# Kernel tuning notes

Hardware: AMD Instinct MI355X
Metric: run time of the kernel (lower is better)

The kernel has to match this reference:

```python
import jax, jax.numpy as jnp
import numpy as np

N = 50000      # nodes
E = 600000     # edges
IN = 128       # in_channels
H = 128        # hidden_channels
CH = 32        # chunk_size
L = 3          # num_layers
G = 64         # num graphs in batch
EPS = 1e-5


def layer_norm(x, gamma, beta):
    mu = jnp.mean(x, axis=-1, keepdims=True)
    var = jnp.mean(jnp.square(x - mu), axis=-1, keepdims=True)
    return (x - mu) * jax.lax.rsqrt(var + EPS) * gamma + beta


def setup_inputs() -> dict:
    key = jax.random.key(0)
    ks = jax.random.split(key, 8)
    x = jax.random.normal(ks[0], (N, IN), dtype=jnp.float32)
    edge_index = jax.random.randint(ks[1], (2, E), 0, N, dtype=jnp.int64)
    batch = jnp.sort(jax.random.randint(ks[2], (N,), 0, G, dtype=jnp.int64))
    W_in = jax.random.normal(ks[3], (IN, H), dtype=jnp.float32) / np.sqrt(IN)
    b_in = jnp.zeros((H,), jnp.float32)
    ln_in_g = jnp.ones((H,), jnp.float32)
    ln_in_b = jnp.zeros((H,), jnp.float32)
    # shared (global_gating=True) tm_net: Linear(2H -> chunk_size)
    W_tm = jax.random.normal(ks[4], (2 * H, CH), dtype=jnp.float32) / np.sqrt(2 * H)
    b_tm = jnp.zeros((CH,), jnp.float32)
    tm_g = jnp.ones((L, H), jnp.float32)   # per-layer tm_norm gamma
    tm_b = jnp.zeros((L, H), jnp.float32)  # per-layer tm_norm beta
    return {"x": x, "edge_index": edge_index, "batch": batch,
            "W_in": W_in, "b_in": b_in, "ln_in_g": ln_in_g, "ln_in_b": ln_in_b,
            "W_tm": W_tm, "b_tm": b_tm, "tm_g": tm_g, "tm_b": tm_b}


def reference(x, edge_index, batch, W_in, b_in, ln_in_g, ln_in_b, W_tm, b_tm, tm_g, tm_b):
    # Input MLP (dropout is identity in eval)
    h = layer_norm(jax.nn.relu(x @ W_in + b_in), ln_in_g, ln_in_b)  # [N,H]

    src, dst = edge_index[0], edge_index[1]
    valid = (src != dst).astype(h.dtype)  # remove self loops
    r = H // CH
    # degree after remove_self_loops + add_self_loops (+1 for the self loop)
    deg = jax.ops.segment_sum(valid, dst, num_segments=N) + 1.0  # [N]

    tm = jnp.zeros((N, CH), h.dtype)  # last_tm_signal
    for j in range(L):
        # scatter-mean message passing with self loops
        msg = h[src] * valid[:, None]                        # [E,H]
        agg = jax.ops.segment_sum(msg, dst, num_segments=N)  # [N,H]
        m = (agg + h) / deg[:, None]
        # ordered gating: softmax -> cumsum -> diff-or with previous signal
        raw = jax.nn.softmax(jnp.concatenate([h, m], axis=1) @ W_tm + b_tm, axis=-1)
        raw = jnp.cumsum(raw, axis=-1)
        raw = tm + (1.0 - tm) * raw                          # [N,CH]
        sig = jnp.repeat(raw, r, axis=1)                     # [N,H]
        h = layer_norm(h * sig + m * (1.0 - sig), tm_g[j], tm_b[j])
        tm = raw

    # global mean pool over graphs
    counts = jax.ops.segment_sum(jnp.ones((N,), h.dtype), batch, num_segments=G)
    pooled = jax.ops.segment_sum(h, batch, num_segments=G) / jnp.maximum(counts, 1.0)[:, None]
    return pooled  # [G,H]
```

## Files before the change

kernel.cpp:

```cpp
#include <hip/hip_runtime.h>

#define NN 50000
#define NE 600000
#define HC 128
#define CHN 32
#define NG 64
#define LN_EPS 1e-5f

typedef unsigned short ushort_t;
typedef unsigned int uint_t;
typedef _Float16 half2_t __attribute__((ext_vector_type(2)));

__device__ __forceinline__ ushort_t f2h(float f) {
    _Float16 h = (_Float16)f;
    return __builtin_bit_cast(ushort_t, h);
}
__device__ __forceinline__ float h2f(ushort_t s) {
    _Float16 h = __builtin_bit_cast(_Float16, s);
    return (float)h;
}
__device__ __forceinline__ uint_t pkh(float e, float o) {
    return (uint_t)f2h(e) | ((uint_t)f2h(o) << 16);
}
__device__ __forceinline__ float dot2h(uint_t a, uint_t b, float c) {
#if __has_builtin(__builtin_amdgcn_fdot2)
    return __builtin_amdgcn_fdot2(__builtin_bit_cast(half2_t, a),
                                  __builtin_bit_cast(half2_t, b), c, false);
#else
    half2_t ha = __builtin_bit_cast(half2_t, a);
    half2_t hb = __builtin_bit_cast(half2_t, b);
    c = fmaf((float)ha.x, (float)hb.x, c);
    c = fmaf((float)ha.y, (float)hb.y, c);
    return c;
#endif
}


__global__ void __launch_bounds__(256) k_hist(const int* __restrict__ ei, int* __restrict__ cnt) {
    int e = blockIdx.x * 256 + threadIdx.x;
    if (e >= NE) return;
    int s = ei[e], d = ei[NE + e];
    if (s != d) atomicAdd(&cnt[d], 1);
}

#define SC_BLOCKS 49

__global__ void __launch_bounds__(256) k_scanA(const int* __restrict__ cnt, int* __restrict__ blocksum) {
    int b = blockIdx.x, t = threadIdx.x;
    int idx = b * 1024 + t * 4;
    int4 v = make_int4(0, 0, 0, 0);
    if (idx + 3 < NN) v = *(const int4*)&cnt[idx];
    else {
        if (idx + 0 < NN) v.x = cnt[idx + 0];
        if (idx + 1 < NN) v.y = cnt[idx + 1];
        if (idx + 2 < NN) v.z = cnt[idx + 2];
        if (idx + 3 < NN) v.w = cnt[idx + 3];
    }
    int s = v.x + v.y + v.z + v.w;
    for (int m = 1; m < 64; m <<= 1) s += __shfl_xor(s, m, 64);
    __shared__ int ws[4];
    if ((t & 63) == 0) ws[t >> 6] = s;
    __syncthreads();
    if (t == 0) blocksum[b] = ws[0] + ws[1] + ws[2] + ws[3];
}

__global__ void __launch_bounds__(64) k_scanB(const int* __restrict__ blocksum, int* __restrict__ blockoff) {
    int t = threadIdx.x;
    int v = (t < SC_BLOCKS) ? blocksum[t] : 0;
    int inc = v;
    for (int d = 1; d < 64; d <<= 1) { int u = __shfl_up(inc, d, 64); if (t >= d) inc += u; }
    if (t < SC_BLOCKS) blockoff[t + 1] = inc;
    if (t == 0) blockoff[0] = 0;
}

__global__ void __launch_bounds__(256) k_scanC(const int* __restrict__ cnt, const int* __restrict__ blockoff,
                                               int* __restrict__ row_ptr) {
    int b = blockIdx.x, t = threadIdx.x;
    int idx = b * 1024 + t * 4;
    int4 v = make_int4(0, 0, 0, 0);
    if (idx + 3 < NN) v = *(const int4*)&cnt[idx];
    else {
        if (idx + 0 < NN) v.x = cnt[idx + 0];
        if (idx + 1 < NN) v.y = cnt[idx + 1];
        if (idx + 2 < NN) v.z = cnt[idx + 2];
        if (idx + 3 < NN) v.w = cnt[idx + 3];
    }
    int s = v.x + v.y + v.z + v.w;
    int lane = t & 63, w = t >> 6;
    int inc = s;
    for (int d = 1; d < 64; d <<= 1) { int u = __shfl_up(inc, d, 64); if (lane >= d) inc += u; }
    __shared__ int wsum[4];
    if (lane == 63) wsum[w] = inc;
    __syncthreads();
    int off = blockoff[b];
    for (int i = 0; i < w; ++i) off += wsum[i];
    int excl = off + inc - s;
    if (idx + 0 < NN) row_ptr[idx + 0] = excl;
    if (idx + 1 < NN) row_ptr[idx + 1] = excl + v.x;
    if (idx + 2 < NN) row_ptr[idx + 2] = excl + v.x + v.y;
    if (idx + 3 < NN) row_ptr[idx + 3] = excl + v.x + v.y + v.z;
    if (b == 0 && t == 0) row_ptr[NN] = blockoff[SC_BLOCKS];
}

__global__ void __launch_bounds__(256) k_fill(const int* __restrict__ ei, const int* __restrict__ row_ptr,
                                              int* __restrict__ fill, int* __restrict__ col) {
    int e = blockIdx.x * 256 + threadIdx.x;
    if (e >= NE) return;
    int s = ei[e], d = ei[NE + e];
    if (s != d) {
        int pos = atomicAdd(&fill[d], 1);
        col[row_ptr[d] + pos] = s;
    }
}


__global__ void __launch_bounds__(256) k_prepW(const float* __restrict__ Wtm, uint_t* __restrict__ Wg) {
    int i = blockIdx.x * 256 + threadIdx.x;
    if (i >= (HC / 2) * 2 * CHN) return;
    int cp = i >> 5, kk = i & 31;
    Wg[i] = pkh(Wtm[(2 * cp) * CHN + kk], Wtm[(2 * cp + 1) * CHN + kk]);
}


#define MLP_NB 8
#define MLP_GROUPS (NN / MLP_NB)

__global__ void __launch_bounds__(256) k_mlp(const float* __restrict__ x, const float* __restrict__ W,
                                             const float* __restrict__ b, const float* __restrict__ g,
                                             const float* __restrict__ be, ushort_t* __restrict__ h2) {
    __shared__ float xs[4][MLP_NB][HC];
    int tid = threadIdx.x;
    int wave = tid >> 6, lane = tid & 63;
    float bx = b[2 * lane],  by = b[2 * lane + 1];
    float gx = g[2 * lane],  gy = g[2 * lane + 1];
    float bex = be[2 * lane], bey = be[2 * lane + 1];
    for (int grp = blockIdx.x * 4 + wave; grp < MLP_GROUPS; grp += gridDim.x * 4) {
        int base = grp * MLP_NB;
        #pragma unroll
        for (int nb = 0; nb < MLP_NB; ++nb) {
            float2 xv = *(const float2*)&x[(size_t)(base + nb) * HC + 2 * lane];
            *(float2*)&xs[wave][nb][2 * lane] = xv;
        }
        float ax[MLP_NB], ay[MLP_NB];
        #pragma unroll
        for (int nb = 0; nb < MLP_NB; ++nb) { ax[nb] = bx; ay[nb] = by; }
        for (int c = 0; c < HC; c += 4) {
            float2 wv0 = *(const float2*)&W[(c + 0) * HC + 2 * lane];
            float2 wv1 = *(const float2*)&W[(c + 1) * HC + 2 * lane];
            float2 wv2 = *(const float2*)&W[(c + 2) * HC + 2 * lane];
            float2 wv3 = *(const float2*)&W[(c + 3) * HC + 2 * lane];
            #pragma unroll
            for (int nb = 0; nb < MLP_NB; ++nb) {
                float4 xv = *(const float4*)&xs[wave][nb][c];
                ax[nb] = fmaf(xv.x, wv0.x, ax[nb]); ay[nb] = fmaf(xv.x, wv0.y, ay[nb]);
                ax[nb] = fmaf(xv.y, wv1.x, ax[nb]); ay[nb] = fmaf(xv.y, wv1.y, ay[nb]);
                ax[nb] = fmaf(xv.z, wv2.x, ax[nb]); ay[nb] = fmaf(xv.z, wv2.y, ay[nb]);
                ax[nb] = fmaf(xv.w, wv3.x, ax[nb]); ay[nb] = fmaf(xv.w, wv3.y, ay[nb]);
            }
        }
        #pragma unroll
        for (int nb = 0; nb < MLP_NB; ++nb) {
            float a0 = fmaxf(ax[nb], 0.f), a1 = fmaxf(ay[nb], 0.f);
            float sm = a0 + a1;
            for (int m = 1; m < 64; m <<= 1) sm += __shfl_xor(sm, m, 64);
            float mu = sm * (1.f / 128.f);
            float d0 = a0 - mu, d1 = a1 - mu;
            float vv = d0 * d0 + d1 * d1;
            for (int m = 1; m < 64; m <<= 1) vv += __shfl_xor(vv, m, 64);
            float inv = rsqrtf(vv * (1.f / 128.f) + LN_EPS);
            float ox = d0 * inv * gx + bex;
            float oy = d1 * inv * gy + bey;
            *(uint_t*)&h2[(size_t)(base + nb) * HC + 2 * lane] = pkh(ox, oy);
        }
    }
}


__global__ void __launch_bounds__(256) k_flayer(
        const ushort_t* __restrict__ h2in, ushort_t* __restrict__ h2out,
        const int* __restrict__ row_ptr, const int* __restrict__ col,
        const uint_t* __restrict__ Wg, const float* __restrict__ btm,
        const float* __restrict__ gall, const float* __restrict__ ball,
        float* __restrict__ tm, int layer) {
    __shared__ uint_t hm_pk[4][2][64];
    int tid = threadIdx.x;
    int wave = tid >> 6, lane = tid & 63;
    int k = lane & 31, half = lane >> 5;
    int node = blockIdx.x * 4 + wave;
    int r0 = row_ptr[node], r1 = row_ptr[node + 1];
    int deg = r1 - r0;
    float tmo = tm[(size_t)node * CHN + k];
    float bk  = btm[k];
    float gx  = gall[layer * HC + 2 * lane], gy  = gall[layer * HC + 2 * lane + 1];
    float bex = ball[layer * HC + 2 * lane], bey = ball[layer * HC + 2 * lane + 1];
    half2_t acc = (half2_t)(_Float16)0;
    for (int base = 0; base < deg; base += 64) {
        int nIdx = min(64, deg - base);
        int myc = (base + lane < deg) ? col[r0 + base + lane] : 0;
        int j = 0;
        for (; j + 4 <= nIdx; j += 4) {
            int s0 = __shfl(myc, j,     64);
            int s1 = __shfl(myc, j + 1, 64);
            int s2 = __shfl(myc, j + 2, 64);
            int s3 = __shfl(myc, j + 3, 64);
            uint_t v0 = *(const uint_t*)&h2in[(size_t)s0 * HC + 2 * lane];
            uint_t v1 = *(const uint_t*)&h2in[(size_t)s1 * HC + 2 * lane];
            uint_t v2 = *(const uint_t*)&h2in[(size_t)s2 * HC + 2 * lane];
            uint_t v3 = *(const uint_t*)&h2in[(size_t)s3 * HC + 2 * lane];
            acc += __builtin_bit_cast(half2_t, v0);
            acc += __builtin_bit_cast(half2_t, v1);
            acc += __builtin_bit_cast(half2_t, v2);
            acc += __builtin_bit_cast(half2_t, v3);
        }
        for (; j < nIdx; ++j) {
            int s = __shfl(myc, j, 64);
            uint_t v = *(const uint_t*)&h2in[(size_t)s * HC + 2 * lane];
            acc += __builtin_bit_cast(half2_t, v);
        }
    }
    float ax = (float)acc.x, ay = (float)acc.y;
    uint_t hvp = *(const uint_t*)&h2in[(size_t)node * HC + 2 * lane];
    float h0 = h2f((ushort_t)(hvp & 0xFFFFu)), h1 = h2f((ushort_t)(hvp >> 16));
    float invdeg = 1.f / (float)(deg + 1);
    float m0 = (ax + h0) * invdeg, m1 = (ay + h1) * invdeg;
    hm_pk[wave][0][lane] = hvp;
    hm_pk[wave][1][lane] = pkh(m0, m1);
    const uint_t* sp = &hm_pk[wave][half][0];
    const uint_t* wp = Wg + (size_t)(half * 64) * CHN + k;
    float z = 0.f;
    #pragma unroll
    for (int i = 0; i < 16; ++i) {
        uint4 s4 = *(const uint4*)&sp[4 * i];
        uint_t w0 = wp[(4 * i + 0) * CHN];
        uint_t w1 = wp[(4 * i + 1) * CHN];
        uint_t w2 = wp[(4 * i + 2) * CHN];
        uint_t w3 = wp[(4 * i + 3) * CHN];
        z = dot2h(s4.x, w0, z);
        z = dot2h(s4.y, w1, z);
        z = dot2h(s4.z, w2, z);
        z = dot2h(s4.w, w3, z);
    }
    z += __shfl_xor(z, 32, 64);
    z += bk;
    float mx = z;
    for (int m = 1; m < 32; m <<= 1) mx = fmaxf(mx, __shfl_xor(mx, m, 32));
    float e = __expf(z - mx);
    float se = e;
    for (int m = 1; m < 32; m <<= 1) se += __shfl_xor(se, m, 32);
    float p = e / se;
    float cum = p;
    for (int d = 1; d < 32; d <<= 1) {
        float t2 = __shfl_up(cum, d, 32);
        if (k >= d) cum += t2;
    }
    float raw = tmo + (1.f - tmo) * cum;
    if (half == 0) tm[(size_t)node * CHN + k] = raw;
    float sig = __shfl(raw, lane >> 1, 64);
    float v0 = h0 * sig + m0 * (1.f - sig);
    float v1 = h1 * sig + m1 * (1.f - sig);
    float sm = v0 + v1;
    for (int m = 1; m < 64; m <<= 1) sm += __shfl_xor(sm, m, 64);
    float mu = sm * (1.f / 128.f);
    float d0 = v0 - mu, d1 = v1 - mu;
    float vv = d0 * d0 + d1 * d1;
    for (int m = 1; m < 64; m <<= 1) vv += __shfl_xor(vv, m, 64);
    float inv = rsqrtf(vv * (1.f / 128.f) + LN_EPS);
    *(uint_t*)&h2out[(size_t)node * HC + 2 * lane] = pkh(d0 * inv * gx + bex,
                                                         d1 * inv * gy + bey);
}


__global__ void __launch_bounds__(1024) k_pool(const ushort_t* __restrict__ h2, const int* __restrict__ batch,
                                               float* __restrict__ out) {
    __shared__ float red[8][HC];
    int g = blockIdx.x;
    int tid = threadIdx.x;
    int c = tid & (HC - 1);
    int w = tid >> 7;
    int a = 0, bnd = NN;
    while (a < bnd) { int mid = (a + bnd) >> 1; if (batch[mid] < g) a = mid + 1; else bnd = mid; }
    int start = a;
    bnd = NN;
    while (a < bnd) { int mid = (a + bnd) >> 1; if (batch[mid] <= g) a = mid + 1; else bnd = mid; }
    int end = a;
    float acc = 0.f;
    for (int n = start + w; n < end; n += 8) acc += h2f(h2[(size_t)n * HC + c]);
    red[w][c] = acc;
    __syncthreads();
    if (w == 0) {
        float s = red[0][c] + red[1][c] + red[2][c] + red[3][c]
                + red[4][c] + red[5][c] + red[6][c] + red[7][c];
        int count = end - start;
        out[g * HC + c] = s / (float)max(count, 1);
    }
}


extern "C" void kernel_launch(void* const* d_in, const int* in_sizes, int n_in,
                              void* d_out, int out_size, void* d_ws, size_t ws_size,
                              hipStream_t stream) {
    const float* x     = (const float*)d_in[0];
    const int*   ei    = (const int*)d_in[1];
    const int*   batch = (const int*)d_in[2];
    const float* W_in  = (const float*)d_in[3];
    const float* b_in  = (const float*)d_in[4];
    const float* g_in  = (const float*)d_in[5];
    const float* be_in = (const float*)d_in[6];
    const float* W_tm  = (const float*)d_in[7];
    const float* b_tm  = (const float*)d_in[8];
    const float* tm_g  = (const float*)d_in[9];
    const float* tm_b  = (const float*)d_in[10];
    float* out = (float*)d_out;

    char* ws = (char*)d_ws;
    int*      cnt = (int*)(ws + 0);
    int*      fil = (int*)(ws + 200000);
    int*      rp  = (int*)(ws + 400000);
    int*      col = (int*)(ws + 600004);
    ushort_t* h2A = (ushort_t*)(ws + 3000064);
    ushort_t* h2B = (ushort_t*)(ws + 15800064);
    float*    tm  = (float*)(ws + 28600064);
    int*      bsum = (int*)(ws + 35000064);
    int*      boff = (int*)(ws + 35000320);
    uint_t*   Wg   = (uint_t*)(ws + 35000576);

    hipMemsetAsync(cnt, 0, 400000, stream);
    hipMemsetAsync(tm, 0, 6400000, stream);

    k_hist<<<(NE + 255) / 256, 256, 0, stream>>>(ei, cnt);
    k_scanA<<<SC_BLOCKS, 256, 0, stream>>>(cnt, bsum);
    k_scanB<<<1, 64, 0, stream>>>(bsum, boff);
    k_scanC<<<SC_BLOCKS, 256, 0, stream>>>(cnt, boff, rp);
    k_fill<<<(NE + 255) / 256, 256, 0, stream>>>(ei, rp, fil, col);
    k_prepW<<<16, 256, 0, stream>>>(W_tm, Wg);

    k_mlp<<<1563, 256, 0, stream>>>(x, W_in, b_in, g_in, be_in, h2A);

    k_flayer<<<NN / 4, 256, 0, stream>>>(h2A, h2B, rp, col, Wg, b_tm, tm_g, tm_b, tm, 0);
    k_flayer<<<NN / 4, 256, 0, stream>>>(h2B, h2A, rp, col, Wg, b_tm, tm_g, tm_b, tm, 1);
    k_flayer<<<NN / 4, 256, 0, stream>>>(h2A, h2B, rp, col, Wg, b_tm, tm_g, tm_b, tm, 2);

    k_pool<<<NG, 1024, 0, stream>>>(h2B, batch, out);
}
```

Baseline: 300.4 us.

## Split wave into two edge halves with 8-byte gathers, fp16 gating state, fused memsets

```diff
diff --git a/kernel.cpp b/kernel.cpp
--- a/kernel.cpp
+++ b/kernel.cpp
@@ -21,6 +21,9 @@
 }
 __device__ __forceinline__ uint_t pkh(float e, float o) {
     return (uint_t)f2h(e) | ((uint_t)f2h(o) << 16);
+}
+__device__ __forceinline__ half2_t bch(uint_t u) {
+    return __builtin_bit_cast(half2_t, u);
 }
 __device__ __forceinline__ float dot2h(uint_t a, uint_t b, float c) {
 #if __has_builtin(__builtin_amdgcn_fdot2)
@@ -114,11 +117,14 @@
 }
 
 
-__global__ void __launch_bounds__(256) k_prepW(const float* __restrict__ Wtm, uint_t* __restrict__ Wg) {
+__global__ void __launch_bounds__(256) k_prep(const float* __restrict__ Wtm, uint_t* __restrict__ Wg,
+                                              int* __restrict__ cnt) {
     int i = blockIdx.x * 256 + threadIdx.x;
-    if (i >= (HC / 2) * 2 * CHN) return;
-    int cp = i >> 5, kk = i & 31;
-    Wg[i] = pkh(Wtm[(2 * cp) * CHN + kk], Wtm[(2 * cp + 1) * CHN + kk]);
+    if (i < 32 * 128) {
+        int cp = i >> 5, kk = i & 31;
+        Wg[i] = pkh(Wtm[(2 * cp) * CHN + kk], Wtm[(2 * cp + 1) * CHN + kk]);
+    }
+    for (int z = i; z < 2 * NN; z += gridDim.x * 256) cnt[z] = 0;
 }
 
 
@@ -127,7 +133,10 @@
 
 __global__ void __launch_bounds__(256) k_mlp(const float* __restrict__ x, const float* __restrict__ W,
                                              const float* __restrict__ b, const float* __restrict__ g,
-                                             const float* __restrict__ be, ushort_t* __restrict__ h2) {
+                                             const float* __restrict__ be, ushort_t* __restrict__ h2,
+                                             ushort_t* __restrict__ tm) {
+    uint_t* tz = (uint_t*)tm;
+    for (int z = blockIdx.x * 256 + threadIdx.x; z < NN * CHN / 2; z += gridDim.x * 256) tz[z] = 0u;
     __shared__ float xs[4][MLP_NB][HC];
     int tid = threadIdx.x;
     int wave = tid >> 6, lane = tid & 63;
@@ -181,52 +190,67 @@
         const int* __restrict__ row_ptr, const int* __restrict__ col,
         const uint_t* __restrict__ Wg, const float* __restrict__ btm,
         const float* __restrict__ gall, const float* __restrict__ ball,
-        float* __restrict__ tm, int layer) {
+        ushort_t* __restrict__ tm, int layer) {
     __shared__ uint_t hm_pk[4][2][64];
     int tid = threadIdx.x;
     int wave = tid >> 6, lane = tid & 63;
-    int k = lane & 31, half = lane >> 5;
+    int l32 = lane & 31, half = lane >> 5;
     int node = blockIdx.x * 4 + wave;
     int r0 = row_ptr[node], r1 = row_ptr[node + 1];
     int deg = r1 - r0;
-    float tmo = tm[(size_t)node * CHN + k];
-    float bk  = btm[k];
-    float gx  = gall[layer * HC + 2 * lane], gy  = gall[layer * HC + 2 * lane + 1];
-    float bex = ball[layer * HC + 2 * lane], bey = ball[layer * HC + 2 * lane + 1];
-    half2_t acc = (half2_t)(_Float16)0;
+    float tmo = h2f(tm[(size_t)node * CHN + l32]);
+    float bk  = btm[l32];
+    float4 gv = *(const float4*)&gall[layer * HC + 4 * l32];
+    float4 bv = *(const float4*)&ball[layer * HC + 4 * l32];
+    half2_t acc0 = (half2_t)(_Float16)0, acc1 = (half2_t)(_Float16)0;
     for (int base = 0; base < deg; base += 64) {
         int nIdx = min(64, deg - base);
         int myc = (base + lane < deg) ? col[r0 + base + lane] : 0;
-        int j = 0;
-        for (; j + 4 <= nIdx; j += 4) {
-            int s0 = __shfl(myc, j,     64);
-            int s1 = __shfl(myc, j + 1, 64);
-            int s2 = __shfl(myc, j + 2, 64);
-            int s3 = __shfl(myc, j + 3, 64);
-            uint_t v0 = *(const uint_t*)&h2in[(size_t)s0 * HC + 2 * lane];
-            uint_t v1 = *(const uint_t*)&h2in[(size_t)s1 * HC + 2 * lane];
-            uint_t v2 = *(const uint_t*)&h2in[(size_t)s2 * HC + 2 * lane];
-            uint_t v3 = *(const uint_t*)&h2in[(size_t)s3 * HC + 2 * lane];
-            acc += __builtin_bit_cast(half2_t, v0);
-            acc += __builtin_bit_cast(half2_t, v1);
-            acc += __builtin_bit_cast(half2_t, v2);
-            acc += __builtin_bit_cast(half2_t, v3);
-        }
-        for (; j < nIdx; ++j) {
-            int s = __shfl(myc, j, 64);
-            uint_t v = *(const uint_t*)&h2in[(size_t)s * HC + 2 * lane];
-            acc += __builtin_bit_cast(half2_t, v);
-        }
-    }
-    float ax = (float)acc.x, ay = (float)acc.y;
-    uint_t hvp = *(const uint_t*)&h2in[(size_t)node * HC + 2 * lane];
-    float h0 = h2f((ushort_t)(hvp & 0xFFFFu)), h1 = h2f((ushort_t)(hvp >> 16));
+        int tmax = (nIdx + 1) >> 1;
+        int t = 0;
+        for (; t + 4 <= tmax; t += 4) {
+            int j0 = 2 * t + half, j1 = j0 + 2, j2 = j0 + 4, j3 = j0 + 6;
+            int s0 = __shfl(myc, j0 & 63, 64);
+            int s1 = __shfl(myc, j1 & 63, 64);
+            int s2 = __shfl(myc, j2 & 63, 64);
+            int s3 = __shfl(myc, j3 & 63, 64);
+            uint2 v0 = *(const uint2*)&h2in[(size_t)s0 * HC + 4 * l32];
+            uint2 v1 = *(const uint2*)&h2in[(size_t)s1 * HC + 4 * l32];
+            uint2 v2 = *(const uint2*)&h2in[(size_t)s2 * HC + 4 * l32];
+            uint2 v3 = *(const uint2*)&h2in[(size_t)s3 * HC + 4 * l32];
+            if (j0 < nIdx) { acc0 += bch(v0.x); acc1 += bch(v0.y); }
+            if (j1 < nIdx) { acc0 += bch(v1.x); acc1 += bch(v1.y); }
+            if (j2 < nIdx) { acc0 += bch(v2.x); acc1 += bch(v2.y); }
+            if (j3 < nIdx) { acc0 += bch(v3.x); acc1 += bch(v3.y); }
+        }
+        for (; t < tmax; ++t) {
+            int j = 2 * t + half;
+            int s = __shfl(myc, j & 63, 64);
+            uint2 v = *(const uint2*)&h2in[(size_t)s * HC + 4 * l32];
+            if (j < nIdx) { acc0 += bch(v.x); acc1 += bch(v.y); }
+        }
+    }
+    {
+        uint_t u0 = __builtin_bit_cast(uint_t, acc0);
+        uint_t u1 = __builtin_bit_cast(uint_t, acc1);
+        acc0 += bch((uint_t)__shfl_xor((int)u0, 32, 64));
+        acc1 += bch((uint_t)__shfl_xor((int)u1, 32, 64));
+    }
+    float a0 = (float)acc0.x, a1 = (float)acc0.y;
+    float a2 = (float)acc1.x, a3 = (float)acc1.y;
+    uint2 hv = *(const uint2*)&h2in[(size_t)node * HC + 4 * l32];
+    float h0 = h2f((ushort_t)(hv.x & 0xFFFFu)), h1 = h2f((ushort_t)(hv.x >> 16));
+    float h2v = h2f((ushort_t)(hv.y & 0xFFFFu)), h3 = h2f((ushort_t)(hv.y >> 16));
     float invdeg = 1.f / (float)(deg + 1);
-    float m0 = (ax + h0) * invdeg, m1 = (ay + h1) * invdeg;
-    hm_pk[wave][0][lane] = hvp;
-    hm_pk[wave][1][lane] = pkh(m0, m1);
+    float m0 = (a0 + h0) * invdeg, m1 = (a1 + h1) * invdeg;
+    float m2 = (a2 + h2v) * invdeg, m3 = (a3 + h3) * invdeg;
+    if (half == 0) {
+        *(uint2*)&hm_pk[wave][0][2 * l32] = hv;
+        uint2 mp; mp.x = pkh(m0, m1); mp.y = pkh(m2, m3);
+        *(uint2*)&hm_pk[wave][1][2 * l32] = mp;
+    }
     const uint_t* sp = &hm_pk[wave][half][0];
-    const uint_t* wp = Wg + (size_t)(half * 64) * CHN + k;
+    const uint_t* wp = Wg + (size_t)(half * 64) * CHN + l32;
     float z = 0.f;
     #pragma unroll
     for (int i = 0; i < 16; ++i) {
@@ -251,22 +275,29 @@
     float cum = p;
     for (int d = 1; d < 32; d <<= 1) {
         float t2 = __shfl_up(cum, d, 32);
-        if (k >= d) cum += t2;
+        if (l32 >= d) cum += t2;
     }
     float raw = tmo + (1.f - tmo) * cum;
-    if (half == 0) tm[(size_t)node * CHN + k] = raw;
-    float sig = __shfl(raw, lane >> 1, 64);
-    float v0 = h0 * sig + m0 * (1.f - sig);
-    float v1 = h1 * sig + m1 * (1.f - sig);
-    float sm = v0 + v1;
-    for (int m = 1; m < 64; m <<= 1) sm += __shfl_xor(sm, m, 64);
+    if (half == 0) tm[(size_t)node * CHN + l32] = f2h(raw);
+    float sig = __shfl(raw, l32, 64);
+    float om = 1.f - sig;
+    float v0 = h0 * sig + m0 * om;
+    float v1 = h1 * sig + m1 * om;
+    float v2 = h2v * sig + m2 * om;
+    float v3 = h3 * sig + m3 * om;
+    float sm = v0 + v1 + v2 + v3;
+    for (int m = 1; m < 32; m <<= 1) sm += __shfl_xor(sm, m, 32);
     float mu = sm * (1.f / 128.f);
-    float d0 = v0 - mu, d1 = v1 - mu;
-    float vv = d0 * d0 + d1 * d1;
-    for (int m = 1; m < 64; m <<= 1) vv += __shfl_xor(vv, m, 64);
+    float d0 = v0 - mu, d1 = v1 - mu, d2 = v2 - mu, d3 = v3 - mu;
+    float vv = d0 * d0 + d1 * d1 + d2 * d2 + d3 * d3;
+    for (int m = 1; m < 32; m <<= 1) vv += __shfl_xor(vv, m, 32);
     float inv = rsqrtf(vv * (1.f / 128.f) + LN_EPS);
-    *(uint_t*)&h2out[(size_t)node * HC + 2 * lane] = pkh(d0 * inv * gx + bex,
-                                                         d1 * inv * gy + bey);
+    if (half == 0) {
+        uint2 o;
+        o.x = pkh(d0 * inv * gv.x + bv.x, d1 * inv * gv.y + bv.y);
+        o.y = pkh(d2 * inv * gv.z + bv.z, d3 * inv * gv.w + bv.w);
+        *(uint2*)&h2out[(size_t)node * HC + 4 * l32] = o;
+    }
 }
 
 
@@ -319,22 +350,19 @@
     int*      col = (int*)(ws + 600004);
     ushort_t* h2A = (ushort_t*)(ws + 3000064);
     ushort_t* h2B = (ushort_t*)(ws + 15800064);
-    float*    tm  = (float*)(ws + 28600064);
+    ushort_t* tm  = (ushort_t*)(ws + 28600064);
     int*      bsum = (int*)(ws + 35000064);
     int*      boff = (int*)(ws + 35000320);
     uint_t*   Wg   = (uint_t*)(ws + 35000576);
 
-    hipMemsetAsync(cnt, 0, 400000, stream);
-    hipMemsetAsync(tm, 0, 6400000, stream);
-
+    k_prep<<<64, 256, 0, stream>>>(W_tm, Wg, cnt);
     k_hist<<<(NE + 255) / 256, 256, 0, stream>>>(ei, cnt);
     k_scanA<<<SC_BLOCKS, 256, 0, stream>>>(cnt, bsum);
     k_scanB<<<1, 64, 0, stream>>>(bsum, boff);
     k_scanC<<<SC_BLOCKS, 256, 0, stream>>>(cnt, boff, rp);
     k_fill<<<(NE + 255) / 256, 256, 0, stream>>>(ei, rp, fil, col);
-    k_prepW<<<16, 256, 0, stream>>>(W_tm, Wg);
-
-    k_mlp<<<1563, 256, 0, stream>>>(x, W_in, b_in, g_in, be_in, h2A);
+
+    k_mlp<<<1563, 256, 0, stream>>>(x, W_in, b_in, g_in, be_in, h2A, tm);
 
     k_flayer<<<NN / 4, 256, 0, stream>>>(h2A, h2B, rp, col, Wg, b_tm, tm_g, tm_b, tm, 0);
     k_flayer<<<NN / 4, 256, 0, stream>>>(h2B, h2A, rp, col, Wg, b_tm, tm_g, tm_b, tm, 1);
```

Measured after the change: 349.8 us. +16.4%, slower.
